# Optimization experiments

Hardware: AMD Instinct MI355X
Metric: run time of the kernel (lower is better)

The kernel has to match this reference:

```python
import jax, jax.numpy as jnp
import numpy as np

NUM_CARDS = 71
NUM_SLOTS = 71
TRUMP_DIM = 7
HIDDEN = [512, 256, 128]
ACTIONS = 9
BATCH = 16384


def setup_inputs() -> dict:
    key = jax.random.key(0)
    ks = jax.random.split(key, 16)
    state_idx = jax.random.randint(ks[0], (BATCH, NUM_SLOTS), 0, NUM_CARDS, dtype=jnp.int32)
    trump_onehot = jax.random.uniform(ks[1], (BATCH, TRUMP_DIM), dtype=jnp.float32)
    legal_mask = jnp.ones((BATCH, ACTIONS), dtype=bool)
    in_dim = NUM_SLOTS * NUM_CARDS + TRUMP_DIM  # 5048
    dims = [in_dim] + HIDDEN
    params = {}
    for i, (d_in, d_out) in enumerate(zip(dims[:-1], dims[1:])):
        params[f"W{i}"] = jax.random.normal(ks[2 + 2 * i], (d_in, d_out), dtype=jnp.float32) * 0.02
        params[f"b{i}"] = jnp.zeros((d_out,), dtype=jnp.float32)
    params["Wp"] = jax.random.normal(ks[10], (dims[-1], ACTIONS), dtype=jnp.float32) * 0.02
    params["bp"] = jnp.zeros((ACTIONS,), dtype=jnp.float32)
    return {"state_idx": state_idx, "trump_onehot": trump_onehot, "legal_mask": legal_mask, **params}


def reference(state_idx, trump_onehot, legal_mask,
              W0, b0, W1, b1, W2, b2, Wp, bp):
    # one-hot encode 71 card slots and flatten: (B, 71*71)
    idx = jnp.clip(state_idx, 0, NUM_CARDS - 1)
    one_hot = jax.nn.one_hot(idx, NUM_CARDS, dtype=jnp.float32)
    flat = one_hot.reshape(one_hot.shape[0], -1)
    x = jnp.concatenate([flat, trump_onehot], axis=1)  # (B, 5048)
    x = jax.nn.relu(x @ W0 + b0)
    x = jax.nn.relu(x @ W1 + b1)
    x = jax.nn.relu(x @ W2 + b2)
    logits = x @ Wp + bp  # (B, 9)
    logits = jnp.where(legal_mask, logits, -jnp.inf)
    return jax.nn.log_softmax(logits, axis=1)
```

## Files before the change

kernel.cpp:

```cpp
#include <hip/hip_runtime.h>
#include <hip/hip_bf16.h>

typedef unsigned int u32;
typedef unsigned short u16;
typedef unsigned char u8;
typedef _Float16 f16;
typedef __attribute__((ext_vector_type(2)))  _Float16 f16x2;
typedef __attribute__((ext_vector_type(8)))  _Float16 f16x8;
typedef __attribute__((ext_vector_type(16))) _Float16 f16x16;
typedef __attribute__((ext_vector_type(4))) float f32x4;

#define NSLOT   71
#define NCARD   71
#define ONEHOT  5041
#define INDIM   5048
#define D0      512
#define D1      256
#define D2      128
#define NACT    9

__device__ __forceinline__ u16 f2h_bits(float x) { f16 h = (f16)x; u16 r; __builtin_memcpy(&r, &h, 2); return r; }

__global__ void prep_kernel(const float* __restrict__ W0, const float* __restrict__ W1,
                            const float* __restrict__ W2,
                            u16* __restrict__ W0h, u16* __restrict__ W1T, u16* __restrict__ W2T) {
    int i = blockIdx.x * 256 + threadIdx.x;
    const int n0 = INDIM * D0;
    const int n1 = D0 * D1;
    const int n2 = D1 * D2;
    if (i < n0) {
        W0h[i] = f2h_bits(W0[i]);
    } else if (i < n0 + n1) {
        int j = i - n0; int n = j >> 9, k = j & 511;
        W1T[j] = f2h_bits(W1[k * D1 + n]);
    } else if (i < n0 + n1 + n2) {
        int j = i - n0 - n1; int n = j >> 8, k = j & 255;
        W2T[j] = f2h_bits(W2[k * D2 + n]);
    }
}

__global__ __launch_bounds__(512)
void layer0_kernel(const int* __restrict__ sidx, const float* __restrict__ trump,
                   const float* __restrict__ b0, const u16* __restrict__ W0h,
                   u16* __restrict__ h0) {
    __shared__ u8 idxl[128 * NSLOT];
    __shared__ float trl[128 * 7];
    const int tid = threadIdx.x;
    const int ct = blockIdx.x & 3;
    const int rbase = (blockIdx.x >> 2) * 128;

    for (int i = tid; i < 128 * NSLOT; i += 512) {
        int v = sidx[rbase * NSLOT + i];
        v = v < 0 ? 0 : (v > NCARD - 1 ? NCARD - 1 : v);
        idxl[i] = (u8)v;
    }
    for (int i = tid; i < 128 * 7; i += 512)
        trl[i] = trump[rbase * 7 + i];
    __syncthreads();

    const int rg = tid >> 3;
    const int cg = tid & 7;
    const int c0 = ct * 128 + cg * 16;
    const u8* ix0 = &idxl[(rg * 2 + 0) * NSLOT];
    const u8* ix1 = &idxl[(rg * 2 + 1) * NSLOT];
    const u16* Wc = W0h + c0;

    f16x16 acc0, acc1;
    {
        f16x16 bias;
        #pragma unroll
        for (int j = 0; j < 16; ++j) bias[j] = (f16)b0[c0 + j];
        acc0 = bias; acc1 = bias;
        #pragma unroll
        for (int t = 0; t < 7; ++t) {
            f16x16 w16 = *(const f16x16*)(Wc + (size_t)(ONEHOT + t) * D0);
            acc0 += w16 * (f16)trl[(rg * 2 + 0) * 7 + t];
            acc1 += w16 * (f16)trl[(rg * 2 + 1) * 7 + t];
        }
    }

#define LD0(s) (*(const f16x16*)(Wc + ((size_t)(s) * NCARD + ix0[(s)]) * D0))
#define LD1(s) (*(const f16x16*)(Wc + ((size_t)(s) * NCARD + ix1[(s)]) * D0))

    f16x16 pa0 = LD0(0), pa1 = LD1(0);
    f16x16 pb0 = LD0(1), pb1 = LD1(1);
    int s = 0;
    for (; s + 3 < NSLOT; s += 2) {
        f16x16 na0 = LD0(s + 2), na1 = LD1(s + 2);
        f16x16 nb0 = LD0(s + 3), nb1 = LD1(s + 3);
        __builtin_amdgcn_sched_barrier(0);
        acc0 += pa0; acc1 += pa1;
        acc0 += pb0; acc1 += pb1;
        pa0 = na0; pa1 = na1; pb0 = nb0; pb1 = nb1;
    }
    {
        f16x16 nc0 = LD0(70), nc1 = LD1(70);
        __builtin_amdgcn_sched_barrier(0);
        acc0 += pa0; acc1 += pa1;
        acc0 += pb0; acc1 += pb1;
        acc0 += nc0; acc1 += nc1;
    }
#undef LD0
#undef LD1

    const f16x16 zero = {};
    f16x16 v0 = __builtin_elementwise_max(acc0, zero);
    f16x16 v1 = __builtin_elementwise_max(acc1, zero);
    uint4* dst0 = (uint4*)(h0 + (size_t)(rbase + rg * 2 + 0) * D0 + c0);
    uint4* dst1 = (uint4*)(h0 + (size_t)(rbase + rg * 2 + 1) * D0 + c0);
    dst0[0] = ((const uint4*)&v0)[0];
    dst0[1] = ((const uint4*)&v0)[1];
    dst1[0] = ((const uint4*)&v1)[0];
    dst1[1] = ((const uint4*)&v1)[1];
}

__global__ __launch_bounds__(512)
void mlp_kernel(const u16* __restrict__ h0, const u16* __restrict__ W1T, const u16* __restrict__ W2T,
                const float* __restrict__ b1, const float* __restrict__ b2,
                const float* __restrict__ Wp, const float* __restrict__ bp,
                const int* __restrict__ legal, float* __restrict__ out) {
    __shared__ u16 Abuf[32 * 520];
    __shared__ u16 h1buf[32 * 264];
    __shared__ u16 h2buf[32 * 136];
    __shared__ float wpb[D2 * NACT + NACT];
    const int tid = threadIdx.x;
    const int r0 = blockIdx.x * 32;

    for (int i = tid; i < 2048; i += 512) {
        int r = i >> 6, g = i & 63;
        uint4 v = *(const uint4*)(h0 + (size_t)(r0 + r) * D0 + g * 8);
        *(uint4*)&Abuf[r * 520 + g * 8] = v;
    }
    for (int i = tid; i < D2 * NACT + NACT; i += 512)
        wpb[i] = (i < D2 * NACT) ? Wp[i] : bp[i - D2 * NACT];
    __syncthreads();

    const int w  = tid >> 6;
    const int l  = tid & 63;
    const int lc = l & 15;
    const int kg = l >> 4;

    {
        const int n0 = w * 32;
        f32x4 a00 = {0.f,0.f,0.f,0.f}, a01 = a00, a10 = a00, a11 = a00;
        for (int kb = 0; kb < D0; kb += 32) {
            f16x8 av0 = *(const f16x8*)&Abuf[lc * 520 + kb + kg * 8];
            f16x8 av1 = *(const f16x8*)&Abuf[(lc + 16) * 520 + kb + kg * 8];
            f16x8 bv0 = *(const f16x8*)(W1T + (size_t)(n0 + lc) * D0 + kb + kg * 8);
            f16x8 bv1 = *(const f16x8*)(W1T + (size_t)(n0 + 16 + lc) * D0 + kb + kg * 8);
            a00 = __builtin_amdgcn_mfma_f32_16x16x32_f16(av0, bv0, a00, 0, 0, 0);
            a01 = __builtin_amdgcn_mfma_f32_16x16x32_f16(av0, bv1, a01, 0, 0, 0);
            a10 = __builtin_amdgcn_mfma_f32_16x16x32_f16(av1, bv0, a10, 0, 0, 0);
            a11 = __builtin_amdgcn_mfma_f32_16x16x32_f16(av1, bv1, a11, 0, 0, 0);
        }
        #pragma unroll
        for (int nb = 0; nb < 2; ++nb) {
            int col = n0 + nb * 16 + lc;
            float bias = b1[col];
            #pragma unroll
            for (int j = 0; j < 4; ++j) {
                f32x4 v0 = nb ? a01 : a00;
                f32x4 v1 = nb ? a11 : a10;
                h1buf[(kg * 4 + j) * 264 + col]        = f2h_bits(fmaxf(v0[j] + bias, 0.f));
                h1buf[(16 + kg * 4 + j) * 264 + col]   = f2h_bits(fmaxf(v1[j] + bias, 0.f));
            }
        }
    }
    __syncthreads();

    {
        const int n0 = w * 16;
        f32x4 c0 = {0.f,0.f,0.f,0.f}, c1 = c0;
        for (int kb = 0; kb < D1; kb += 32) {
            f16x8 av0 = *(const f16x8*)&h1buf[lc * 264 + kb + kg * 8];
            f16x8 av1 = *(const f16x8*)&h1buf[(lc + 16) * 264 + kb + kg * 8];
            f16x8 bv  = *(const f16x8*)(W2T + (size_t)(n0 + lc) * D1 + kb + kg * 8);
            c0 = __builtin_amdgcn_mfma_f32_16x16x32_f16(av0, bv, c0, 0, 0, 0);
            c1 = __builtin_amdgcn_mfma_f32_16x16x32_f16(av1, bv, c1, 0, 0, 0);
        }
        int col = n0 + lc;
        float bias = b2[col];
        #pragma unroll
        for (int j = 0; j < 4; ++j) {
            h2buf[(kg * 4 + j) * 136 + col]      = f2h_bits(fmaxf(c0[j] + bias, 0.f));
            h2buf[(16 + kg * 4 + j) * 136 + col] = f2h_bits(fmaxf(c1[j] + bias, 0.f));
        }
    }
    __syncthreads();

    if (tid < 128) {
        int r = tid >> 2, q = tid & 3;
        float part[NACT];
        #pragma unroll
        for (int a = 0; a < NACT; ++a) part[a] = 0.f;
        int kbase = q * 32;
        #pragma unroll
        for (int kk = 0; kk < 32; kk += 2) {
            u32 pr = *(const u32*)&h2buf[r * 136 + kbase + kk];
            f16x2 hp; __builtin_memcpy(&hp, &pr, 4);
            float x0 = (float)hp.x, x1 = (float)hp.y;
            #pragma unroll
            for (int a = 0; a < NACT; ++a)
                part[a] += x0 * wpb[(kbase + kk) * NACT + a] + x1 * wpb[(kbase + kk + 1) * NACT + a];
        }
        #pragma unroll
        for (int a = 0; a < NACT; ++a) {
            part[a] += __shfl_xor(part[a], 1, 64);
            part[a] += __shfl_xor(part[a], 2, 64);
        }
        if (q == 0) {
            int row = r0 + r;
            const int* mk = legal + (size_t)row * NACT;
            float lg[NACT]; float mx = -INFINITY;
            #pragma unroll
            for (int a = 0; a < NACT; ++a) {
                lg[a] = part[a] + wpb[D2 * NACT + a];
                if (mk[a] != 0 && lg[a] > mx) mx = lg[a];
            }
            float s = 0.f;
            #pragma unroll
            for (int a = 0; a < NACT; ++a) if (mk[a] != 0) s += __expf(lg[a] - mx);
            float lse = mx + __logf(s);
            #pragma unroll
            for (int a = 0; a < NACT; ++a)
                out[(size_t)row * NACT + a] = (mk[a] != 0) ? (lg[a] - lse) : -INFINITY;
        }
    }
}

extern "C" void kernel_launch(void* const* d_in, const int* in_sizes, int n_in,
                              void* d_out, int out_size, void* d_ws, size_t ws_size,
                              hipStream_t stream) {
    const int*   sidx  = (const int*)d_in[0];
    const float* trump = (const float*)d_in[1];
    const int*   legal = (const int*)d_in[2];
    const float* W0 = (const float*)d_in[3];
    const float* b0 = (const float*)d_in[4];
    const float* W1 = (const float*)d_in[5];
    const float* b1 = (const float*)d_in[6];
    const float* W2 = (const float*)d_in[7];
    const float* b2 = (const float*)d_in[8];
    const float* Wp = (const float*)d_in[9];
    const float* bp = (const float*)d_in[10];
    float* out = (float*)d_out;

    u16* W0h  = (u16*)d_ws;
    u16* W1T  = W0h + (size_t)INDIM * D0;
    u16* W2T  = W1T + (size_t)D0 * D1;
    u16* h0   = W2T + (size_t)D1 * D2;

    const int total = INDIM * D0 + D0 * D1 + D1 * D2;
    prep_kernel<<<(total + 255) / 256, 256, 0, stream>>>(W0, W1, W2, W0h, W1T, W2T);
    layer0_kernel<<<512, 512, 0, stream>>>(sidx, trump, b0, W0h, h0);
    mlp_kernel<<<512, 512, 0, stream>>>(h0, W1T, W2T, b1, b2, Wp, bp, legal, out);
}
```

Baseline: 84.48 us.

## Process 64 rows per MLP block and load layer-1 activations directly from global

The MLP kernel now handles 64 batch rows per block instead of 32, halving the grid. Each loaded W1/W2 fragment is reused across four row tiles, which halves weight traffic from L2. The LDS staging of h0 and its barrier are removed, so A fragments are read straight from global memory. The trade-off is fewer blocks, 256 on a GPU with many CUs, and more register pressure from eight accumulators.

```diff
diff --git a/kernel.cpp b/kernel.cpp
--- a/kernel.cpp
+++ b/kernel.cpp
@@ -119,21 +119,14 @@
                 const float* __restrict__ b1, const float* __restrict__ b2,
                 const float* __restrict__ Wp, const float* __restrict__ bp,
                 const int* __restrict__ legal, float* __restrict__ out) {
-    __shared__ u16 Abuf[32 * 520];
-    __shared__ u16 h1buf[32 * 264];
-    __shared__ u16 h2buf[32 * 136];
+    __shared__ u16 h1buf[64 * 264];
+    __shared__ u16 h2buf[64 * 136];
     __shared__ float wpb[D2 * NACT + NACT];
     const int tid = threadIdx.x;
-    const int r0 = blockIdx.x * 32;
-
-    for (int i = tid; i < 2048; i += 512) {
-        int r = i >> 6, g = i & 63;
-        uint4 v = *(const uint4*)(h0 + (size_t)(r0 + r) * D0 + g * 8);
-        *(uint4*)&Abuf[r * 520 + g * 8] = v;
-    }
+    const int r0 = blockIdx.x * 64;
+
     for (int i = tid; i < D2 * NACT + NACT; i += 512)
         wpb[i] = (i < D2 * NACT) ? Wp[i] : bp[i - D2 * NACT];
-    __syncthreads();
 
     const int w  = tid >> 6;
     const int l  = tid & 63;
@@ -142,53 +135,56 @@
 
     {
         const int n0 = w * 32;
-        f32x4 a00 = {0.f,0.f,0.f,0.f}, a01 = a00, a10 = a00, a11 = a00;
+        f32x4 acc[4][2] = {};
+        const u16* a_base  = h0  + (size_t)(r0 + lc) * D0;
+        const u16* b_base0 = W1T + (size_t)(n0 + lc) * D0;
+        const u16* b_base1 = W1T + (size_t)(n0 + 16 + lc) * D0;
         for (int kb = 0; kb < D0; kb += 32) {
-            f16x8 av0 = *(const f16x8*)&Abuf[lc * 520 + kb + kg * 8];
-            f16x8 av1 = *(const f16x8*)&Abuf[(lc + 16) * 520 + kb + kg * 8];
-            f16x8 bv0 = *(const f16x8*)(W1T + (size_t)(n0 + lc) * D0 + kb + kg * 8);
-            f16x8 bv1 = *(const f16x8*)(W1T + (size_t)(n0 + 16 + lc) * D0 + kb + kg * 8);
-            a00 = __builtin_amdgcn_mfma_f32_16x16x32_f16(av0, bv0, a00, 0, 0, 0);
-            a01 = __builtin_amdgcn_mfma_f32_16x16x32_f16(av0, bv1, a01, 0, 0, 0);
-            a10 = __builtin_amdgcn_mfma_f32_16x16x32_f16(av1, bv0, a10, 0, 0, 0);
-            a11 = __builtin_amdgcn_mfma_f32_16x16x32_f16(av1, bv1, a11, 0, 0, 0);
+            f16x8 bv0 = *(const f16x8*)(b_base0 + kb + kg * 8);
+            f16x8 bv1 = *(const f16x8*)(b_base1 + kb + kg * 8);
+            #pragma unroll
+            for (int m = 0; m < 4; ++m) {
+                f16x8 av = *(const f16x8*)(a_base + (size_t)m * 16 * D0 + kb + kg * 8);
+                acc[m][0] = __builtin_amdgcn_mfma_f32_16x16x32_f16(av, bv0, acc[m][0], 0, 0, 0);
+                acc[m][1] = __builtin_amdgcn_mfma_f32_16x16x32_f16(av, bv1, acc[m][1], 0, 0, 0);
+            }
         }
         #pragma unroll
         for (int nb = 0; nb < 2; ++nb) {
             int col = n0 + nb * 16 + lc;
             float bias = b1[col];
             #pragma unroll
-            for (int j = 0; j < 4; ++j) {
-                f32x4 v0 = nb ? a01 : a00;
-                f32x4 v1 = nb ? a11 : a10;
-                h1buf[(kg * 4 + j) * 264 + col]        = f2h_bits(fmaxf(v0[j] + bias, 0.f));
-                h1buf[(16 + kg * 4 + j) * 264 + col]   = f2h_bits(fmaxf(v1[j] + bias, 0.f));
+            for (int m = 0; m < 4; ++m)
+                #pragma unroll
+                for (int j = 0; j < 4; ++j)
+                    h1buf[(m * 16 + kg * 4 + j) * 264 + col] = f2h_bits(fmaxf(acc[m][nb][j] + bias, 0.f));
+        }
+    }
+    __syncthreads();
+
+    {
+        const int n0 = w * 16;
+        f32x4 acc[4] = {};
+        const u16* b_base = W2T + (size_t)(n0 + lc) * D1;
+        for (int kb = 0; kb < D1; kb += 32) {
+            f16x8 bv = *(const f16x8*)(b_base + kb + kg * 8);
+            #pragma unroll
+            for (int m = 0; m < 4; ++m) {
+                f16x8 av = *(const f16x8*)&h1buf[(m * 16 + lc) * 264 + kb + kg * 8];
+                acc[m] = __builtin_amdgcn_mfma_f32_16x16x32_f16(av, bv, acc[m], 0, 0, 0);
             }
-        }
-    }
-    __syncthreads();
-
-    {
-        const int n0 = w * 16;
-        f32x4 c0 = {0.f,0.f,0.f,0.f}, c1 = c0;
-        for (int kb = 0; kb < D1; kb += 32) {
-            f16x8 av0 = *(const f16x8*)&h1buf[lc * 264 + kb + kg * 8];
-            f16x8 av1 = *(const f16x8*)&h1buf[(lc + 16) * 264 + kb + kg * 8];
-            f16x8 bv  = *(const f16x8*)(W2T + (size_t)(n0 + lc) * D1 + kb + kg * 8);
-            c0 = __builtin_amdgcn_mfma_f32_16x16x32_f16(av0, bv, c0, 0, 0, 0);
-            c1 = __builtin_amdgcn_mfma_f32_16x16x32_f16(av1, bv, c1, 0, 0, 0);
         }
         int col = n0 + lc;
         float bias = b2[col];
         #pragma unroll
-        for (int j = 0; j < 4; ++j) {
-            h2buf[(kg * 4 + j) * 136 + col]      = f2h_bits(fmaxf(c0[j] + bias, 0.f));
-            h2buf[(16 + kg * 4 + j) * 136 + col] = f2h_bits(fmaxf(c1[j] + bias, 0.f));
-        }
+        for (int m = 0; m < 4; ++m)
+            #pragma unroll
+            for (int j = 0; j < 4; ++j)
+                h2buf[(m * 16 + kg * 4 + j) * 136 + col] = f2h_bits(fmaxf(acc[m][j] + bias, 0.f));
     }
     __syncthreads();
 
-    if (tid < 128) {
+    if (tid < 256) {
         int r = tid >> 2, q = tid & 3;
         float part[NACT];
         #pragma unroll
@@ -252,5 +248,5 @@
     const int total = INDIM * D0 + D0 * D1 + D1 * D2;
     prep_kernel<<<(total + 255) / 256, 256, 0, stream>>>(W0, W1, W2, W0h, W1T, W2T);
     layer0_kernel<<<512, 512, 0, stream>>>(sidx, trump, b0, W0h, h0);
-    mlp_kernel<<<512, 512, 0, stream>>>(h0, W1T, W2T, b1, b2, Wp, bp, legal, out);
-}
+    mlp_kernel<<<256, 512, 0, stream>>>(h0, W1T, W2T, b1, b2, Wp, bp, legal, out);
+}
```

Measured after the change: 91.25 us. 8.0% more time.
